# Kernel optimization log

Measured on AMD Instinct MI355X. Metric: run time of the kernel, lower is better.

## Reference

```python
import jax, jax.numpy as jnp
import numpy as np

ALPHA = 0.2  # LeakyReLU negative slope
NEG_BIG = jnp.float32(-9e15)


def _leaky_relu(x):
    return jnp.where(x > 0, x, ALPHA * x)


def gat_layer(h, adj, w, a):
    """One GATLayer with concat=True (ELU output), dropout=0 (eval mode).
    h: [N, F_in], adj: [N, N] int, w: [F_in, F_out], a: [2*F_out, 1].
    """
    Wh = h @ w                         # [N, F_out]
    f_out = w.shape[1]
    Wh1 = Wh @ a[:f_out]               # [N, 1]
    Wh2 = Wh @ a[f_out:]               # [N, 1]
    e = _leaky_relu(Wh1 + Wh2.T)       # [N, N] dense additive scores
    att = jnp.where(adj > 0, e, NEG_BIG)
    att = jax.nn.softmax(att, axis=1)  # row softmax
    return jax.nn.elu(att @ Wh)        # [N, F_out]


def setup_inputs() -> dict:
    N, F_IN, H, NHEADS = 4096, 128, 64, 4
    key = jax.random.key(0)
    ks = jax.random.split(key, 9)
    s = jnp.float32(0.1)  # keep logits in a sane range
    x = jax.random.normal(ks[0], (N, F_IN), jnp.float32)
    adj = jax.random.randint(ks[1], (N, N), 0, 2, jnp.int32)
    return {
        "x": x,
        "adj": adj,
        "w_heads": jax.random.normal(ks[2], (NHEADS, F_IN, H), jnp.float32) * s,
        "a_heads": jax.random.normal(ks[3], (NHEADS, 2 * H, 1), jnp.float32) * s,
        "w_out": jax.random.normal(ks[4], (NHEADS * H, H), jnp.float32) * s,
        "a_out": jax.random.normal(ks[5], (2 * H, 1), jnp.float32) * s,
        "lin_w": jax.random.normal(ks[6], (H, F_IN), jnp.float32) * s,
        "lin_b": jnp.zeros((H,), jnp.float32),
        "outlin_w": jax.random.normal(ks[7], (H, H), jnp.float32) * s,
        "outlin_b": jnp.zeros((H,), jnp.float32),
    }


def reference(x, adj, w_heads, a_heads, w_out, a_out, lin_w, lin_b, outlin_w, outlin_b):
    N = x.shape[0]
    x_residual = x @ lin_w.T + lin_b                      # nn.Linear(input, hidden)
    # multi-head GAT layers, concatenated along features
    heads = jax.vmap(gat_layer, in_axes=(None, None, 0, 0))(x, adj, w_heads, a_heads)  # [nh, N, H]
    hcat = jnp.transpose(heads, (1, 0, 2)).reshape(N, -1)  # [N, nh*H]
    out = gat_layer(hcat, adj, w_out, a_out)               # out_att (concat=True => ELU)
    out = (x_residual + out) @ outlin_w.T + outlin_b       # out_linear
    return jax.nn.elu(out)
```

## Files before the change

kernel.cpp:

```cpp
#include <hip/hip_runtime.h>
#include <hip/hip_bf16.h>
#include <stdint.h>

#define F_IN 128
#define H 64
#define NH 4
#define KCH_H 8
#define KCH_O 16
#define LOG2E 1.44269504088896f

typedef __attribute__((ext_vector_type(8))) short bf16x8;
typedef __attribute__((ext_vector_type(4))) float floatx4;

static __device__ __forceinline__ unsigned short f2bf(float v) {
    __hip_bfloat16 b = __float2bfloat16(v);
    return *(unsigned short*)&b;
}
static __device__ __forceinline__ float bf2f(unsigned short u) {
    return __uint_as_float((unsigned int)u << 16);
}

__global__ void pack_adjp_kernel(const int* __restrict__ adj,
                                 unsigned char* __restrict__ adjp,
                                 int N, int KT) {
    int it = blockIdx.x;
    int half = blockIdx.y;
    int i0 = it * 16;
    int tid = threadIdx.x;
    int n = tid & 15, q = (tid >> 4) & 3, w = tid >> 6;
    const int* row = adj + (size_t)(i0 + n) * N;
    unsigned char* dst = adjp + (size_t)it * KT * 64;
    int ktbase = half * (KT / 2) + w;
#pragma unroll 4
    for (int j = 0; j < KT / 8; ++j) {
        int kt = ktbase + 4 * j;
        int c0 = kt * 32 + q * 8;
        int4 a = *(const int4*)(row + c0);
        int4 b = *(const int4*)(row + c0 + 4);
        unsigned byte =
            (unsigned)(a.x > 0) | ((unsigned)(a.y > 0) << 1) |
            ((unsigned)(a.z > 0) << 2) | ((unsigned)(a.w > 0) << 3) |
            ((unsigned)(b.x > 0) << 4) | ((unsigned)(b.y > 0) << 5) |
            ((unsigned)(b.z > 0) << 6) | ((unsigned)(b.w > 0) << 7);
        dst[kt * 64 + q * 16 + n] = (unsigned char)byte;
    }
}

__global__ void wh_fused_kernel(const float* __restrict__ x,
                                const float* __restrict__ w_heads,
                                const float* __restrict__ a_heads,
                                const float* __restrict__ lin_w,
                                const float* __restrict__ lin_b,
                                unsigned short* __restrict__ Bpk,
                                float* __restrict__ x_res,
                                float* __restrict__ s1h,
                                float* __restrict__ s2h, int N) {
    int tid = threadIdx.x;
    int h = tid >> 6, f = tid & 63;
    int i0 = blockIdx.x * 8;
    int KT = N >> 5;
    __shared__ float xs[8][F_IN];
    for (int e = tid; e < 8 * F_IN; e += 256)
        xs[e >> 7][e & 127] = x[(size_t)(i0 + (e >> 7)) * F_IN + (e & 127)];
    __syncthreads();
    float acc[8];
#pragma unroll
    for (int r = 0; r < 8; ++r) acc[r] = 0.f;
    float xr0 = 0.f, xr1 = 0.f;
    const float* w = w_heads + (size_t)h * F_IN * H + f;
    const float* lw = lin_w + (size_t)f * F_IN;
#pragma unroll 4
    for (int k = 0; k < F_IN; ++k) {
        float wv = w[(size_t)k * H];
#pragma unroll
        for (int r = 0; r < 8; ++r) acc[r] += xs[r][k] * wv;
        float wx = lw[k];
        xr0 += xs[h][k] * wx;
        xr1 += xs[h + 4][k] * wx;
    }
    {
        int kt = i0 >> 5, qq = (i0 >> 3) & 3;
        union { unsigned short s[8]; uint4 v; } t;
#pragma unroll
        for (int r = 0; r < 8; ++r) t.s[r] = f2bf(acc[r]);
        unsigned short* d = Bpk +
            (((size_t)(h * KT + kt) * 4 + (f >> 4)) * 64 + qq * 16 + (f & 15)) * 8;
        *(uint4*)d = t.v;
    }
    float b = lin_b[f];
    x_res[(size_t)(i0 + h) * H + f] = xr0 + b;
    x_res[(size_t)(i0 + h + 4) * H + f] = xr1 + b;
    float a1v = a_heads[(size_t)h * 2 * H + f];
    float a2v = a_heads[(size_t)h * 2 * H + H + f];
#pragma unroll
    for (int r = 0; r < 8; ++r) {
        float t1 = acc[r] * a1v;
        float t2 = acc[r] * a2v;
#pragma unroll
        for (int off = 32; off > 0; off >>= 1) {
            t1 += __shfl_xor(t1, off, 64);
            t2 += __shfl_xor(t2, off, 64);
        }
        if (f == 0) {
            s1h[(size_t)h * N + i0 + r] = t1 * LOG2E;
            s2h[(size_t)h * N + i0 + r] = t2 * LOG2E;
        }
    }
}

template <int KTC>
__global__ __launch_bounds__(256, 8)
void pv2_kernel(const unsigned char* __restrict__ adjp,
                const unsigned short* __restrict__ Bpk,
                const float* __restrict__ s1a,
                const float* __restrict__ s2a,
                unsigned short* __restrict__ outp, float* __restrict__ lp,
                int out_stride, int N) {
    const int h = blockIdx.y, z = blockIdx.z;
    const int KT = N >> 5;
    const int kt0 = z * KTC;
    const int tid = threadIdx.x;
    const int wave = tid >> 6, lane = tid & 63;
    const int n = lane & 15, q = lane >> 4;
    const int i0w = (blockIdx.x * 4 + wave) * 16;

    __shared__ float s2s[KTC * 32];
    __shared__ unsigned short ldsB[2][2048];

    const float4* s2src = (const float4*)(s2a + (size_t)h * N + kt0 * 32);
    for (int e = tid; e < KTC * 8; e += 256) ((float4*)s2s)[e] = s2src[e];

    const unsigned short* Bb = Bpk + ((size_t)h * KT + kt0) * 2048;
    uint4 breg = *(const uint4*)(Bb + tid * 8);
    *(uint4*)&ldsB[0][tid * 8] = breg;
    breg = *(const uint4*)(Bb + 2048 + tid * 8);

    const unsigned char* ap = adjp + ((size_t)(i0w >> 4) * KT + kt0) * 64 + lane;
    unsigned int a_c = ap[0];
    unsigned int a_n = ap[64];
    const float s1v = s1a[(size_t)h * N + i0w + n];

    floatx4 acc[4];
    floatx4 accl = {0.f, 0.f, 0.f, 0.f};
#pragma unroll
    for (int g = 0; g < 4; ++g) acc[g] = (floatx4){0.f, 0.f, 0.f, 0.f};

    bf16x8 ones;
    {
        short one = (n == 0) ? (short)0x3F80 : (short)0;
#pragma unroll
        for (int jj = 0; jj < 8; ++jj) ones[jj] = one;
    }

    __syncthreads();

#pragma unroll 2
    for (int k = 0; k < KTC; ++k) {
        if (k + 1 < KTC) *(uint4*)&ldsB[(k + 1) & 1][tid * 8] = breg;
        unsigned int a_2 = 0;
        if (k + 2 < KTC) {
            breg = *(const uint4*)(Bb + (size_t)(k + 2) * 2048 + tid * 8);
            a_2 = ap[(size_t)(k + 2) * 64];
        }

        float4 sa = *(const float4*)&s2s[k * 32 + q * 8];
        float4 sb = *(const float4*)&s2s[k * 32 + q * 8 + 4];
        const float* sv = (const float*)&sa;
        const float* sw = (const float*)&sb;
        float e[8];
#pragma unroll
        for (int jj = 0; jj < 8; ++jj) {
            float sj = (jj < 4 ? sv[jj] : sw[jj - 4]);
            float tt = s1v + sj;
            float lr = fmaxf(tt, 0.2f * tt);
            lr = (a_c & (1u << jj)) ? lr : -150.f;
            e[jj] = __builtin_amdgcn_exp2f(lr);
        }
        union { unsigned int u[4]; bf16x8 v; } u;
        u.u[0] = __builtin_amdgcn_perm(__float_as_uint(e[1]), __float_as_uint(e[0]), 0x07060302u);
        u.u[1] = __builtin_amdgcn_perm(__float_as_uint(e[3]), __float_as_uint(e[2]), 0x07060302u);
        u.u[2] = __builtin_amdgcn_perm(__float_as_uint(e[5]), __float_as_uint(e[4]), 0x07060302u);
        u.u[3] = __builtin_amdgcn_perm(__float_as_uint(e[7]), __float_as_uint(e[6]), 0x07060302u);

        bf16x8 bf0 = *(const bf16x8*)&ldsB[k & 1][0 * 512 + lane * 8];
        bf16x8 bf1 = *(const bf16x8*)&ldsB[k & 1][1 * 512 + lane * 8];
        bf16x8 bf2 = *(const bf16x8*)&ldsB[k & 1][2 * 512 + lane * 8];
        bf16x8 bf3 = *(const bf16x8*)&ldsB[k & 1][3 * 512 + lane * 8];

        acc[0] = __builtin_amdgcn_mfma_f32_16x16x32_bf16(u.v, bf0, acc[0], 0, 0, 0);
        acc[1] = __builtin_amdgcn_mfma_f32_16x16x32_bf16(u.v, bf1, acc[1], 0, 0, 0);
        acc[2] = __builtin_amdgcn_mfma_f32_16x16x32_bf16(u.v, bf2, acc[2], 0, 0, 0);
        acc[3] = __builtin_amdgcn_mfma_f32_16x16x32_bf16(u.v, bf3, acc[3], 0, 0, 0);
        accl   = __builtin_amdgcn_mfma_f32_16x16x32_bf16(u.v, ones, accl, 0, 0, 0);

        a_c = a_n;
        a_n = a_2;
        __syncthreads();
    }

    unsigned short* obase = outp + ((size_t)z * N + i0w) * out_stride + h * 64;
#pragma unroll
    for (int r = 0; r < 4; ++r) {
        int rr = q * 4 + r;
        unsigned short* op = obase + (size_t)rr * out_stride + n;
        op[0]  = f2bf(acc[0][r]);
        op[16] = f2bf(acc[1][r]);
        op[32] = f2bf(acc[2][r]);
        op[48] = f2bf(acc[3][r]);
    }
    if (n == 0) {
        float* lrow = lp + ((size_t)z * gridDim.y + h) * N + i0w;
#pragma unroll
        for (int r = 0; r < 4; ++r) lrow[q * 4 + r] = accl[r];
    }
}

__global__ void whout2_kernel(const unsigned short* __restrict__ hcp,
                              const float* __restrict__ lhp,
                              const float* __restrict__ w_out,
                              const float* __restrict__ a_out,
                              unsigned short* __restrict__ BpkO,
                              float* __restrict__ s1o,
                              float* __restrict__ s2o, int N) {
    int tid = threadIdx.x;
    int i0 = blockIdx.x * 8;
    int KT = N >> 5;
    __shared__ float hs[8][256];
    __shared__ float linv[8][NH];
    if (tid < 8 * NH) {
        int r = tid >> 2, hd = tid & 3;
        float l = 0.f;
#pragma unroll
        for (int p = 0; p < KCH_H; ++p)
            l += lhp[((size_t)p * NH + hd) * N + i0 + r];
        linv[r][hd] = 1.f / fmaxf(l, 1e-30f);
    }
    __syncthreads();
    const size_t ps = (size_t)N * 256;
    for (int e = tid; e < 8 * 256; e += 256) {
        int r = e >> 8, k = e & 255;
        size_t off = (size_t)(i0 + r) * 256 + k;
        float v = 0.f;
#pragma unroll
        for (int p = 0; p < KCH_H; ++p) v += bf2f(hcp[p * ps + off]);
        v *= linv[r][k >> 6];
        hs[r][k] = v > 0.f ? v : expm1f(v);
    }
    __syncthreads();
    int f = tid & 63, rl = tid >> 6;
    float a0 = 0.f, a1 = 0.f;
#pragma unroll 4
    for (int k = 0; k < 256; ++k) {
        float wv = w_out[(size_t)k * H + f];
        a0 += hs[rl][k] * wv;
        a1 += hs[rl + 4][k] * wv;
    }
    float w1 = a_out[f], w2 = a_out[H + f];
    float t10 = a0 * w1, t20 = a0 * w2, t11 = a1 * w1, t21 = a1 * w2;
#pragma unroll
    for (int off = 32; off > 0; off >>= 1) {
        t10 += __shfl_xor(t10, off, 64);
        t20 += __shfl_xor(t20, off, 64);
        t11 += __shfl_xor(t11, off, 64);
        t21 += __shfl_xor(t21, off, 64);
    }
    if (f == 0) {
        s1o[i0 + rl] = t10 * LOG2E;
        s2o[i0 + rl] = t20 * LOG2E;
        s1o[i0 + rl + 4] = t11 * LOG2E;
        s2o[i0 + rl + 4] = t21 * LOG2E;
    }
    __syncthreads();
    float* wsW = &hs[0][0];
    wsW[rl * 64 + f] = a0;
    wsW[(rl + 4) * 64 + f] = a1;
    __syncthreads();
    if (tid < 64) {
        int kt = i0 >> 5, qq = (i0 >> 3) & 3;
        int g = tid >> 4, nn = tid & 15;
        union { unsigned short s[8]; uint4 v; } t;
#pragma unroll
        for (int r = 0; r < 8; ++r) t.s[r] = f2bf(wsW[r * 64 + g * 16 + nn]);
        unsigned short* d = BpkO +
            (((size_t)kt * 4 + g) * 64 + qq * 16 + nn) * 8;
        *(uint4*)d = t.v;
    }
}

__global__ void final2_kernel(const unsigned short* __restrict__ o2p,
                              const float* __restrict__ lop,
                              const float* __restrict__ x_res,
                              const float* __restrict__ outlin_w,
                              const float* __restrict__ outlin_b,
                              float* __restrict__ out, int N) {
    int tid = threadIdx.x;
    int f = tid & 63, rl = tid >> 6;
    int i0 = blockIdx.x * 8;
    __shared__ float hs[8][H];
    __shared__ float linv[8];
    if (tid < 8) {
        float l = 0.f;
#pragma unroll
        for (int p = 0; p < KCH_O; ++p) l += lop[(size_t)p * N + i0 + tid];
        linv[tid] = 1.f / fmaxf(l, 1e-30f);
    }
    __syncthreads();
    const size_t ps = (size_t)N * 64;
    for (int e = tid; e < 8 * 64; e += 256) {
        int r = e >> 6, ff = e & 63;
        size_t off = (size_t)(i0 + r) * 64 + ff;
        float v = 0.f;
#pragma unroll
        for (int p = 0; p < KCH_O; ++p) v += bf2f(o2p[p * ps + off]);
        v *= linv[r];
        v = v > 0.f ? v : expm1f(v);
        hs[r][ff] = v + x_res[off];
    }
    __syncthreads();
    float b = outlin_b[f];
    float a0 = b, a1 = b;
#pragma unroll 8
    for (int k = 0; k < H; ++k) {
        float wv = outlin_w[(size_t)f * H + k];
        a0 += hs[rl][k] * wv;
        a1 += hs[rl + 4][k] * wv;
    }
    a0 = a0 > 0.f ? a0 : expm1f(a0);
    a1 = a1 > 0.f ? a1 : expm1f(a1);
    out[(size_t)(i0 + rl) * H + f] = a0;
    out[(size_t)(i0 + rl + 4) * H + f] = a1;
}

extern "C" void kernel_launch(void* const* d_in, const int* in_sizes, int n_in,
                              void* d_out, int out_size, void* d_ws, size_t ws_size,
                              hipStream_t stream) {
    const float* x        = (const float*)d_in[0];
    const int*   adj      = (const int*)d_in[1];
    const float* w_heads  = (const float*)d_in[2];
    const float* a_heads  = (const float*)d_in[3];
    const float* w_out    = (const float*)d_in[4];
    const float* a_out    = (const float*)d_in[5];
    const float* lin_w    = (const float*)d_in[6];
    const float* lin_b    = (const float*)d_in[7];
    const float* outlin_w = (const float*)d_in[8];
    const float* outlin_b = (const float*)d_in[9];
    float* out = (float*)d_out;

    const int N = in_sizes[0] / F_IN;
    const int KT = N >> 5;

    char* p = (char*)d_ws;
    unsigned short* part = (unsigned short*)p;  p += (size_t)KCH_H * N * 256 * 2;
    float* x_res  = (float*)p;  p += (size_t)N * 64 * 4;
    float* s1h    = (float*)p;  p += (size_t)NH * N * 4;
    float* s2h    = (float*)p;  p += (size_t)NH * N * 4;
    float* s1o    = (float*)p;  p += (size_t)N * 4;
    float* s2o    = (float*)p;  p += (size_t)N * 4;
    float* lh_part = (float*)p; p += (size_t)KCH_H * NH * N * 4;
    float* lo_part = (float*)p; p += (size_t)KCH_O * N * 4;
    unsigned short* Bpk  = (unsigned short*)p;  p += (size_t)NH * KT * 2048 * 2;
    unsigned short* BpkO = (unsigned short*)p;  p += (size_t)KT * 2048 * 2;
    unsigned char* adjp  = (unsigned char*)p;   p += (size_t)(N / 16) * KT * 64;

    pack_adjp_kernel<<<dim3(N / 16, 2), 256, 0, stream>>>(adj, adjp, N, KT);
    wh_fused_kernel<<<N / 8, 256, 0, stream>>>(x, w_heads, a_heads, lin_w, lin_b,
                                               Bpk, x_res, s1h, s2h, N);
    pv2_kernel<16><<<dim3(N / 64, NH, KCH_H), 256, 0, stream>>>(
        adjp, Bpk, s1h, s2h, part, lh_part, NH * H, N);
    whout2_kernel<<<N / 8, 256, 0, stream>>>(part, lh_part, w_out, a_out,
                                             BpkO, s1o, s2o, N);
    pv2_kernel<8><<<dim3(N / 64, 1, KCH_O), 256, 0, stream>>>(
        adjp, BpkO, s1o, s2o, part, lo_part, H, N);
    final2_kernel<<<N / 8, 256, 0, stream>>>(part, lo_part, x_res, outlin_w, outlin_b, out, N);
}
```

Baseline: 202.4 us.

## Fuse adjacency packing with Wh projection and double K-split of attention kernels

Merges the adjacency bit-packing kernel and the Wh/residual projection kernel into one launch, with pack work split into finer blocks. The lin_w matrix is staged transposed in shared memory for coalesced access. The split-K factor of both attention passes is doubled (with half the tiles per chunk) to expose more parallelism. This costs larger partial buffers, more reduction work downstream and extra shared memory per projection block.

After: 195.9 us. -3.2%, faster.

```diff
diff --git a/kernel.cpp b/kernel.cpp
--- a/kernel.cpp
+++ b/kernel.cpp
@@ -5,8 +5,8 @@
 #define F_IN 128
 #define H 64
 #define NH 4
-#define KCH_H 8
-#define KCH_O 16
+#define KCH_H 16
+#define KCH_O 32
 #define LOG2E 1.44269504088896f
 
 typedef __attribute__((ext_vector_type(8))) short bf16x8;
@@ -20,61 +20,68 @@
     return __uint_as_float((unsigned int)u << 16);
 }
 
-__global__ void pack_adjp_kernel(const int* __restrict__ adj,
-                                 unsigned char* __restrict__ adjp,
-                                 int N, int KT) {
-    int it = blockIdx.x;
-    int half = blockIdx.y;
-    int i0 = it * 16;
-    int tid = threadIdx.x;
-    int n = tid & 15, q = (tid >> 4) & 3, w = tid >> 6;
-    const int* row = adj + (size_t)(i0 + n) * N;
-    unsigned char* dst = adjp + (size_t)it * KT * 64;
-    int ktbase = half * (KT / 2) + w;
-#pragma unroll 4
-    for (int j = 0; j < KT / 8; ++j) {
-        int kt = ktbase + 4 * j;
-        int c0 = kt * 32 + q * 8;
-        int4 a = *(const int4*)(row + c0);
-        int4 b = *(const int4*)(row + c0 + 4);
-        unsigned byte =
-            (unsigned)(a.x > 0) | ((unsigned)(a.y > 0) << 1) |
-            ((unsigned)(a.z > 0) << 2) | ((unsigned)(a.w > 0) << 3) |
-            ((unsigned)(b.x > 0) << 4) | ((unsigned)(b.y > 0) << 5) |
-            ((unsigned)(b.z > 0) << 6) | ((unsigned)(b.w > 0) << 7);
-        dst[kt * 64 + q * 16 + n] = (unsigned char)byte;
-    }
-}
-
-__global__ void wh_fused_kernel(const float* __restrict__ x,
-                                const float* __restrict__ w_heads,
-                                const float* __restrict__ a_heads,
-                                const float* __restrict__ lin_w,
-                                const float* __restrict__ lin_b,
-                                unsigned short* __restrict__ Bpk,
-                                float* __restrict__ x_res,
-                                float* __restrict__ s1h,
-                                float* __restrict__ s2h, int N) {
-    int tid = threadIdx.x;
+__global__ void prep_kernel(const int* __restrict__ adj,
+                            unsigned char* __restrict__ adjp,
+                            const float* __restrict__ x,
+                            const float* __restrict__ w_heads,
+                            const float* __restrict__ a_heads,
+                            const float* __restrict__ lin_w,
+                            const float* __restrict__ lin_b,
+                            unsigned short* __restrict__ Bpk,
+                            float* __restrict__ x_res,
+                            float* __restrict__ s1h,
+                            float* __restrict__ s2h, int N) {
+    const int bid = blockIdx.x;
+    const int tid = threadIdx.x;
+    const int KT = N >> 5;
+    const int WH_BLOCKS = N / 8;
+
+    if (bid >= WH_BLOCKS) {
+        int idx = bid - WH_BLOCKS;
+        int it = idx >> 3, rem = idx & 7, half = rem >> 2, zz = rem & 3;
+        int i0 = it * 16;
+        int n = tid & 15, q = (tid >> 4) & 3, w = tid >> 6;
+        const int* row = adj + (size_t)(i0 + n) * N;
+        unsigned char* dst = adjp + (size_t)it * KT * 64;
+        int ktbase = half * (KT / 2) + zz * 16 + w;
+#pragma unroll
+        for (int j = 0; j < 4; ++j) {
+            int kt = ktbase + 4 * j;
+            int c0 = kt * 32 + q * 8;
+            int4 a = *(const int4*)(row + c0);
+            int4 b = *(const int4*)(row + c0 + 4);
+            unsigned byte =
+                (unsigned)(a.x > 0) | ((unsigned)(a.y > 0) << 1) |
+                ((unsigned)(a.z > 0) << 2) | ((unsigned)(a.w > 0) << 3) |
+                ((unsigned)(b.x > 0) << 4) | ((unsigned)(b.y > 0) << 5) |
+                ((unsigned)(b.z > 0) << 6) | ((unsigned)(b.w > 0) << 7);
+            dst[kt * 64 + q * 16 + n] = (unsigned char)byte;
+        }
+        return;
+    }
+
     int h = tid >> 6, f = tid & 63;
-    int i0 = blockIdx.x * 8;
-    int KT = N >> 5;
+    int i0 = bid * 8;
     __shared__ float xs[8][F_IN];
+    __shared__ float lwT[F_IN][65];
     for (int e = tid; e < 8 * F_IN; e += 256)
         xs[e >> 7][e & 127] = x[(size_t)(i0 + (e >> 7)) * F_IN + (e & 127)];
+    for (int e = tid; e < 64 * F_IN; e += 256) {
+        int ff = e >> 7, k = e & 127;
+        lwT[k][ff] = lin_w[e];
+    }
     __syncthreads();
     float acc[8];
 #pragma unroll
     for (int r = 0; r < 8; ++r) acc[r] = 0.f;
     float xr0 = 0.f, xr1 = 0.f;
     const float* w = w_heads + (size_t)h * F_IN * H + f;
-    const float* lw = lin_w + (size_t)f * F_IN;
 #pragma unroll 4
     for (int k = 0; k < F_IN; ++k) {
         float wv = w[(size_t)k * H];
 #pragma unroll
         for (int r = 0; r < 8; ++r) acc[r] += xs[r][k] * wv;
-        float wx = lw[k];
+        float wx = lwT[k][f];
         xr0 += xs[h][k] * wx;
         xr1 += xs[h + 4][k] * wx;
     }
@@ -362,14 +369,13 @@
     unsigned short* BpkO = (unsigned short*)p;  p += (size_t)KT * 2048 * 2;
     unsigned char* adjp  = (unsigned char*)p;   p += (size_t)(N / 16) * KT * 64;
 
-    pack_adjp_kernel<<<dim3(N / 16, 2), 256, 0, stream>>>(adj, adjp, N, KT);
-    wh_fused_kernel<<<N / 8, 256, 0, stream>>>(x, w_heads, a_heads, lin_w, lin_b,
-                                               Bpk, x_res, s1h, s2h, N);
-    pv2_kernel<16><<<dim3(N / 64, NH, KCH_H), 256, 0, stream>>>(
+    prep_kernel<<<N / 8 + (N / 16) * 8, 256, 0, stream>>>(
+        adj, adjp, x, w_heads, a_heads, lin_w, lin_b, Bpk, x_res, s1h, s2h, N);
+    pv2_kernel<8><<<dim3(N / 64, NH, KCH_H), 256, 0, stream>>>(
         adjp, Bpk, s1h, s2h, part, lh_part, NH * H, N);
     whout2_kernel<<<N / 8, 256, 0, stream>>>(part, lh_part, w_out, a_out,
                                              BpkO, s1o, s2o, N);
-    pv2_kernel<8><<<dim3(N / 64, 1, KCH_O), 256, 0, stream>>>(
+    pv2_kernel<4><<<dim3(N / 64, 1, KCH_O), 256, 0, stream>>>(
         adjp, BpkO, s1o, s2o, part, lo_part, H, N);
     final2_kernel<<<N / 8, 256, 0, stream>>>(part, lo_part, x_res, outlin_w, outlin_b, out, N);
 }
```
